# Kernel tuning notes

Measured on AMD Instinct MI355X. Metric: run time of the kernel, lower is better.

## Reference

```python
import jax, jax.numpy as jnp
import numpy as np
from math import sqrt

D_MODEL = 1024
HEADS = 16
D_K = D_MODEL // HEADS
NEG = -1e9


def setup_inputs() -> dict:
    key = jax.random.key(0)
    ks = jax.random.split(key, 8)
    bs, s, d = 2, 2048, D_MODEL
    inp = {
        "k": jax.random.normal(ks[0], (bs, s, d), jnp.float32),
        "v": jax.random.normal(ks[1], (bs, s, d), jnp.float32),
        "q": jax.random.normal(ks[2], (bs, s, d), jnp.float32),
        "mask": jax.random.randint(ks[3], (bs, s, 1), 0, 2).astype(jnp.int64),
        # torch nn.Linear weights: y = x @ W.T, W is [out, in]
        "Wq": jax.random.normal(ks[4], (d, d), jnp.float32) / sqrt(d),
        "Wk": jax.random.normal(ks[5], (d, d), jnp.float32) / sqrt(d),
        "Wv": jax.random.normal(ks[6], (d, d), jnp.float32) / sqrt(d),
        "Wo": jax.random.normal(ks[7], (d, d), jnp.float32) / sqrt(d),
    }
    return inp


def reference(k, v, q, mask, Wq, Wk, Wv, Wo):
    bs, s_k, d = k.shape
    s_q = q.shape[1]
    h, d_k = HEADS, D_K
    # linear projections (no bias), then split heads -> [bs, h, s, d_k]
    kh = (k @ Wk.T).reshape(bs, s_k, h, d_k).transpose(0, 2, 1, 3)
    vh = (v @ Wv.T).reshape(bs, s_k, h, d_k).transpose(0, 2, 1, 3)
    qh = (q @ Wq.T).reshape(bs, s_q, h, d_k).transpose(0, 2, 1, 3)
    # scaled dot-product scores [bs, h, s_q, s_k]
    scores = jnp.einsum("bhqd,bhkd->bhqk", qh, kh) / sqrt(d_k)
    # mask [bs, s_k, 1] -> [bs, 1, 1, s_k], masked positions get -1e9
    m = mask[:, None].transpose(0, 1, 3, 2)  # [bs,1,1,s_k]
    scores = jnp.where(m == 0, NEG, scores)
    probs = jax.nn.softmax(scores, axis=-1)  # dropout is identity (eval)
    attn = jnp.einsum("bhqk,bhkd->bhqd", probs, vh)
    attn_concat = attn.transpose(0, 2, 1, 3).reshape(bs, s_q, d)
    return attn_concat @ Wo.T
```

## Files before the change

### kernel.cpp

```cpp
#include <hip/hip_runtime.h>

typedef __bf16 bf16x8 __attribute__((ext_vector_type(8)));
typedef float f32x4 __attribute__((ext_vector_type(4)));

#define BS 2
#define SEQ 2048
#define DM 1024
#define NH 16
#define DKH 64
#define GM 4096
#define GN 1024
#define GK 1024
#define NEGV (-1e9f)

#define OFF_XQ 0u
#define OFF_XK 4194304u
#define OFF_XV 8388608u
#define OFF_WQ 12582912u
#define OFF_WK 13631488u
#define OFF_WV 14680064u
#define OFF_WO 15728640u
#define OFF_QH 16777216u
#define OFF_KC 20971520u
#define OFF_VT 25165824u
#define OFF_AT OFF_XQ

#if __has_builtin(__builtin_amdgcn_exp2f)
#define EXP2(x) __builtin_amdgcn_exp2f(x)
#else
static __device__ __forceinline__ float EXP2(float x) {
    float r;
    asm volatile("v_exp_f32 %0, %1" : "=v"(r) : "v"(x));
    return r;
}
#endif

__device__ __forceinline__ unsigned cvt_pk(float lo, float hi) {
    unsigned r;
    asm volatile("v_cvt_pk_bf16_f32 %0, %1, %2" : "=v"(r) : "v"(lo), "v"(hi));
    return r;
}

__device__ __forceinline__ unsigned short f2b(float f) {
    unsigned u = __builtin_bit_cast(unsigned, f);
    u += 0x7fffu + ((u >> 16) & 1u);
    return (unsigned short)(u >> 16);
}

typedef const __attribute__((address_space(1))) unsigned int* gas_t;
typedef __attribute__((address_space(3))) unsigned int* las_t;

__device__ __forceinline__ void gload_lds16(const ushort* g, ushort* l) {
    __builtin_amdgcn_global_load_lds((gas_t)(const void*)g, (las_t)(void*)l, 16, 0, 0);
}

__global__ __launch_bounds__(256)
void cvt_kernel(const float* __restrict__ q, const float* __restrict__ k,
                const float* __restrict__ v, const float* __restrict__ wq,
                const float* __restrict__ wk, const float* __restrict__ wv,
                const float* __restrict__ wo, ushort* __restrict__ ws)
{
    const float* src; unsigned n; unsigned dst;
    switch (blockIdx.y) {
        case 0: src = q;  n = 4194304u; dst = OFF_XQ; break;
        case 1: src = k;  n = 4194304u; dst = OFF_XK; break;
        case 2: src = v;  n = 4194304u; dst = OFF_XV; break;
        case 3: src = wq; n = 1048576u; dst = OFF_WQ; break;
        case 4: src = wk; n = 1048576u; dst = OFF_WK; break;
        case 5: src = wv; n = 1048576u; dst = OFF_WV; break;
        default: src = wo; n = 1048576u; dst = OFF_WO; break;
    }
    unsigned i = (blockIdx.x * 256u + threadIdx.x) * 4u;
    if (i >= n) return;
    float4 f = *(const float4*)(src + i);
    ushort4 o;
    o.x = f2b(f.x); o.y = f2b(f.y); o.z = f2b(f.z); o.w = f2b(f.w);
    *(ushort4*)(ws + dst + i) = o;
}

__global__ __launch_bounds__(256)
void scan_kernel(const int* __restrict__ mask, int* __restrict__ cpos, int* __restrict__ mbuf)
{
    const int b = blockIdx.x;
    const int* mp = mask + (size_t)b * SEQ;
    const int tid = threadIdx.x;
    const int lane = tid & 63, w = tid >> 6;
    int v[8];
    int cnt = 0;
#pragma unroll
    for (int j = 0; j < 8; ++j) { v[j] = mp[tid * 8 + j]; cnt += (v[j] != 0); }
    int inc = cnt;
#pragma unroll
    for (int d = 1; d < 64; d <<= 1) {
        int t = __shfl_up(inc, d);
        if (lane >= d) inc += t;
    }
    __shared__ int wsum[4];
    if (lane == 63) wsum[w] = inc;
    __syncthreads();
    int base = inc - cnt;
    for (int i = 0; i < w; ++i) base += wsum[i];
    int c = base;
    int* ob = cpos + (size_t)b * SEQ;
#pragma unroll
    for (int j = 0; j < 8; ++j) {
        ob[tid * 8 + j] = (v[j] != 0) ? c : -1;
        c += (v[j] != 0);
    }
    if (tid == 255) mbuf[b] = base + cnt;
}

template<bool PROJ>
__global__ __launch_bounds__(256)
void gemm_bt(const ushort* __restrict__ Abase, const ushort* __restrict__ Bbase,
             ushort* __restrict__ wsbase, float* __restrict__ of,
             const int* __restrict__ cpos)
{
    __shared__ __align__(16) ushort lA[128 * 64];
    __shared__ __align__(16) ushort lB[128 * 64];

    const ushort* A = Abase;
    const ushort* Bw = Bbase;
    float scale = 1.0f;
    if (PROJ) {
        unsigned z = blockIdx.z;
        A  += (size_t)z * (GM * GK);
        Bw += (size_t)z * (GN * GK);
        if (z == 0) scale = 0.125f * 1.44269504088896f;
    }

    const int tid = threadIdx.x;
    const int lane = tid & 63, wid = tid >> 6;
    const int wr = wid >> 1, wc = wid & 1;
    const int lr = lane & 15, lg = lane >> 4;
    const int lin = blockIdx.y * 8 + blockIdx.x;
    const int swz = (lin & 7) * 32 + (lin >> 3);
    const int m0 = (swz >> 3) * 128, n0 = (swz & 7) * 128;
    const int srow = wid * 32 + (lane >> 3);
    const int scol = (lane & 7) * 8;

    f32x4 acc[4][4] = {};

    for (int k0 = 0; k0 < GK; k0 += 64) {
        __syncthreads();
#pragma unroll
        for (int p = 0; p < 4; ++p) {
            gload_lds16(A + (size_t)(m0 + srow + p * 8) * GK + k0 + scol,
                        &lA[(wid * 32 + p * 8) * 64]);
            gload_lds16(Bw + (size_t)(n0 + srow + p * 8) * GK + k0 + scol,
                        &lB[(wid * 32 + p * 8) * 64]);
        }
        __syncthreads();
#pragma unroll
        for (int kk = 0; kk < 2; ++kk) {
            bf16x8 af[4], bfr[4];
#pragma unroll
            for (int i = 0; i < 4; ++i) {
                af[i]  = *(const bf16x8*)(&lA[(wr * 64 + i * 16 + lr) * 64 + kk * 32 + lg * 8]);
                bfr[i] = *(const bf16x8*)(&lB[(wc * 64 + i * 16 + lr) * 64 + kk * 32 + lg * 8]);
            }
#pragma unroll
            for (int i = 0; i < 4; ++i)
#pragma unroll
                for (int j = 0; j < 4; ++j)
                    acc[i][j] = __builtin_amdgcn_mfma_f32_16x16x32_bf16(af[i], bfr[j], acc[i][j], 0, 0, 0);
        }
    }

    if (PROJ) {
        const int z = blockIdx.z;
        ushort* qh = wsbase + OFF_QH;
        ushort* kc = wsbase + OFF_KC;
        ushort* vtp = wsbase + OFF_VT;
#pragma unroll
        for (int i = 0; i < 4; ++i) {
#pragma unroll
            for (int r = 0; r < 4; ++r) {
                int row = m0 + wr * 64 + i * 16 + lg * 4 + r;
                int b = row >> 11, s = row & 2047;
                if (z == 0) {
#pragma unroll
                    for (int j = 0; j < 4; ++j) {
                        int col = n0 + wc * 64 + j * 16 + lr;
                        qh[(((size_t)b * NH + (col >> 6)) * SEQ + s) * DKH + (col & 63)] =
                            f2b(acc[i][j][r] * scale);
                    }
                } else {
                    int c = cpos[b * SEQ + s];
                    if (c >= 0) {
                        if (z == 1) {
#pragma unroll
                            for (int j = 0; j < 4; ++j) {
                                int col = n0 + wc * 64 + j * 16 + lr;
                                kc[(((size_t)b * NH + (col >> 6)) * SEQ + c) * DKH + (col & 63)] =
                                    f2b(acc[i][j][r]);
                            }
                        } else {
                            int vt = (c & ~63) | ((c & 15) * 4 + ((c >> 4) & 3));
#pragma unroll
                            for (int j = 0; j < 4; ++j) {
                                int col = n0 + wc * 64 + j * 16 + lr;
                                vtp[(((size_t)b * NH + (col >> 6)) * DKH + (col & 63)) * SEQ + vt] =
                                    f2b(acc[i][j][r]);
                            }
                        }
                    }
                }
            }
        }
    } else {
#pragma unroll
        for (int i = 0; i < 4; ++i)
#pragma unroll
            for (int j = 0; j < 4; ++j) {
                int col = n0 + wc * 64 + j * 16 + lr;
#pragma unroll
                for (int r = 0; r < 4; ++r) {
                    int row = m0 + wr * 64 + i * 16 + lg * 4 + r;
                    of[(size_t)row * GN + col] = acc[i][j][r];
                }
            }
    }
}

__global__ __launch_bounds__(256)
void attn_kernel(ushort* __restrict__ ws, const int* __restrict__ mbuf)
{
    const int bid = blockIdx.x;
    const int qt = bid & 31;
    const int h  = (bid >> 5) & 15;
    const int b  = bid >> 9;
    const int bh = b * NH + h;

    const ushort* Qp = ws + OFF_QH + (size_t)bh * (SEQ * DKH);
    const ushort* Kc = ws + OFF_KC + (size_t)bh * (SEQ * DKH);
    const ushort* VT = ws + OFF_VT + (size_t)bh * (DKH * SEQ);
    ushort* At = ws + OFF_AT;

    const int mb = mbuf[b];
    const int nt = (mb + 63) >> 6;

    __shared__ __align__(16) ushort lK[2][64 * 64];
    __shared__ __align__(16) ushort lV[2][64 * 64];
    __shared__ __align__(16) ushort lP[4][16][72];

    const int tid = threadIdx.x;
    const int lane = tid & 63, wid = tid >> 6;
    const int lr = lane & 15, lg = lane >> 4;
    ushort* lPw = &lP[wid][0][0];

    const int srow = wid * 16 + (lane >> 3);
    const int sg = lane & 7;

    const int qrow0 = qt * 64 + wid * 16;
    bf16x8 qf[2];
#pragma unroll
    for (int kk = 0; kk < 2; ++kk)
        qf[kk] = *(const bf16x8*)(Qp + (size_t)(qrow0 + lr) * DKH + kk * 32 + lg * 8);

    f32x4 acc_o[4] = {};
    float lrun[4] = {0.f, 0.f, 0.f, 0.f};

    auto STAGE = [&](int buf, int kt) {
        const int kbase = kt * 64;
#pragma unroll
        for (int c = 0; c < 2; ++c) {
            int r = srow + c * 8;
            gload_lds16(Kc + (size_t)(kbase + r) * DKH + ((sg ^ (r & 7)) * 8),
                        &lK[buf][(wid * 16 + c * 8) * 64]);
            gload_lds16(VT + (size_t)r * SEQ + kbase + ((sg ^ (r & 7)) * 8),
                        &lV[buf][(wid * 16 + c * 8) * 64]);
        }
    };

    STAGE(0, 0);
    __syncthreads();

    for (int kt = 0; kt < nt; ++kt) {
        const int cur = kt & 1;
        if (kt + 1 < nt) STAGE(cur ^ 1, kt + 1);
        const ushort* lKc = lK[cur];
        const ushort* lVc = lV[cur];

        f32x4 s[4];
        __builtin_amdgcn_s_setprio(1);
#pragma unroll
        for (int fc = 0; fc < 4; ++fc) {
            int row = fc * 16 + lr;
            int sw = row & 7;
            bf16x8 kf0 = *(const bf16x8*)(lKc + row * 64 + ((lg ^ sw) * 8));
            bf16x8 kf1 = *(const bf16x8*)(lKc + row * 64 + (((4 + lg) ^ sw) * 8));
            f32x4 t = {};
            t = __builtin_amdgcn_mfma_f32_16x16x32_bf16(qf[0], kf0, t, 0, 0, 0);
            t = __builtin_amdgcn_mfma_f32_16x16x32_bf16(qf[1], kf1, t, 0, 0, 0);
            s[fc] = t;
        }
        __builtin_amdgcn_s_setprio(0);

        if (kt == nt - 1) {
            const int kbase = kt * 64;
#pragma unroll
            for (int fc = 0; fc < 4; ++fc)
                if (kbase + fc * 16 + lr >= mb)
                    s[fc] = f32x4{NEGV, NEGV, NEGV, NEGV};
        }

#pragma unroll
        for (int r = 0; r < 4; ++r) {
            float p0 = EXP2(s[0][r]), p1 = EXP2(s[1][r]);
            float p2 = EXP2(s[2][r]), p3 = EXP2(s[3][r]);
            lrun[r] += (p0 + p1) + (p2 + p3);
            uint2 pk;
            pk.x = cvt_pk(p0, p1);
            pk.y = cvt_pk(p2, p3);
            *(uint2*)(lPw + (lg * 4 + r) * 72 + lr * 4) = pk;
        }

        __builtin_amdgcn_s_setprio(1);
#pragma unroll
        for (int kk = 0; kk < 2; ++kk) {
            bf16x8 pf = *(const bf16x8*)(lPw + lr * 72 + kk * 32 + lg * 8);
#pragma unroll
            for (int fc2 = 0; fc2 < 4; ++fc2) {
                int d = fc2 * 16 + lr;
                bf16x8 vf = *(const bf16x8*)(lVc + d * 64 + (((kk * 4 + lg) ^ (d & 7)) * 8));
                acc_o[fc2] = __builtin_amdgcn_mfma_f32_16x16x32_bf16(pf, vf, acc_o[fc2], 0, 0, 0);
            }
        }
        __builtin_amdgcn_s_setprio(0);
        __syncthreads();
    }

#pragma unroll
    for (int r = 0; r < 4; ++r) {
        float l = lrun[r];
        l += __shfl_xor(l, 1);
        l += __shfl_xor(l, 2);
        l += __shfl_xor(l, 4);
        l += __shfl_xor(l, 8);
        float rl = 1.0f / l;
        int qrow = qrow0 + lg * 4 + r;
#pragma unroll
        for (int fc2 = 0; fc2 < 4; ++fc2)
            At[((size_t)(b * SEQ) + qrow) * DM + h * DKH + fc2 * 16 + lr] =
                f2b(acc_o[fc2][r] * rl);
    }
}

extern "C" void kernel_launch(void* const* d_in, const int* in_sizes, int n_in,
                              void* d_out, int out_size, void* d_ws, size_t ws_size,
                              hipStream_t stream) {
    const float* kin = (const float*)d_in[0];
    const float* vin = (const float*)d_in[1];
    const float* qin = (const float*)d_in[2];
    const int*   msk = (const int*)d_in[3];
    const float* wq  = (const float*)d_in[4];
    const float* wk  = (const float*)d_in[5];
    const float* wv  = (const float*)d_in[6];
    const float* wo  = (const float*)d_in[7];
    ushort* ws = (ushort*)d_ws;
    float* out = (float*)d_out;
    int* cposb = (int*)d_out;
    int* mbuf = cposb + BS * SEQ;

    scan_kernel<<<2, 256, 0, stream>>>(msk, cposb, mbuf);
    cvt_kernel<<<dim3(4096, 7), 256, 0, stream>>>(qin, kin, vin, wq, wk, wv, wo, ws);
    gemm_bt<true><<<dim3(8, 32, 3), 256, 0, stream>>>(ws + OFF_XQ, ws + OFF_WQ, ws, nullptr, cposb);
    attn_kernel<<<1024, 256, 0, stream>>>(ws, mbuf);
    gemm_bt<false><<<dim3(8, 32, 1), 256, 0, stream>>>(ws + OFF_AT, ws + OFF_WO, ws, out, nullptr);
}
```

Before: 141.1 us.

## Replace QKV projection GEMM with 256x256 double-buffered swizzled-LDS pipelined kernel

The batched Q/K/V projection GEMM moves from a 128x128-tile, 256-thread kernel with a single LDS buffer to a 256x256-tile, 512-thread kernel. The new kernel double-buffers LDS, XOR-swizzles the LDS layout to avoid bank conflicts, interleaves global-to-LDS loads with MFMA quadrants under explicit barriers and vmcnt waits, raises wave priority around MFMAs, and remaps blocks per XCD. The goal is to hide load latency and increase operand reuse in the largest GEMM. The cost is much higher LDS and register use per block, only 192 blocks in the grid, and a hand-tuned schedule that depends on the exact order of vmcnt waits.

Measured after the change: 138.3 us. -2.0%, faster.

```diff
diff --git a/kernel.cpp b/kernel.cpp
--- a/kernel.cpp
+++ b/kernel.cpp
@@ -53,6 +53,9 @@
 __device__ __forceinline__ void gload_lds16(const ushort* g, ushort* l) {
     __builtin_amdgcn_global_load_lds((gas_t)(const void*)g, (las_t)(void*)l, 16, 0, 0);
 }
+
+#define BARRIER() do { __builtin_amdgcn_s_barrier(); __builtin_amdgcn_sched_barrier(0); } while (0)
+#define VMCNT(n) do { asm volatile("s_waitcnt vmcnt(" #n ")" ::: "memory"); __builtin_amdgcn_sched_barrier(0); } while (0)
 
 __global__ __launch_bounds__(256)
 void cvt_kernel(const float* __restrict__ q, const float* __restrict__ k,
@@ -110,24 +113,167 @@
     if (tid == 255) mbuf[b] = base + cnt;
 }
 
-template<bool PROJ>
+__global__ __launch_bounds__(512)
+void gemm256(const ushort* __restrict__ Abase, const ushort* __restrict__ Bbase,
+             ushort* __restrict__ wsbase, const int* __restrict__ cpos)
+{
+    __shared__ __align__(16) ushort lA[2][2][8192];
+    __shared__ __align__(16) ushort lB[2][2][8192];
+
+    const unsigned z = blockIdx.z;
+    const ushort* A  = Abase + (size_t)z * (GM * GK);
+    const ushort* Bw = Bbase + (size_t)z * (GN * GK);
+    const float scale = (z == 0) ? 0.125f * 1.44269504088896f : 1.0f;
+
+    const int tid = threadIdx.x;
+    const int lane = tid & 63, wid = tid >> 6;
+    const int wr = wid >> 2, wc = wid & 3;
+    const int lr = lane & 15, lg = lane >> 4;
+    const int srow8 = lane >> 3, scol = lane & 7;
+
+    const int lin = blockIdx.y * 4 + blockIdx.x;
+    const int xcd = lin & 7, kidx = lin >> 3;
+    const int m0 = (xcd * 2 + (kidx >> 2)) * 256;
+    const int n0 = (kidx & 3) * 256;
+
+    f32x4 acc[8][4] = {};
+    bf16x8 aq[4][2], aq2[4][2], b01[2][2], b23[2][2];
+
+#define STAGE_A(s, h, t)                                                          \
+    _Pragma("unroll") for (int c = 0; c < 2; ++c) {                               \
+        int rih = (wid * 2 + c) * 8 + srow8;                                      \
+        gload_lds16(A + (size_t)(m0 + (h) * 128 + rih) * GK + (t) * 64 +          \
+                        ((scol ^ (rih & 7)) * 8),                                 \
+                    &lA[s][h][(wid * 2 + c) * 512]);                              \
+    }
+#define STAGE_B(s, h, t)                                                          \
+    _Pragma("unroll") for (int c = 0; c < 2; ++c) {                               \
+        int rih = (wid * 2 + c) * 8 + srow8;                                      \
+        gload_lds16(Bw + (size_t)(n0 + (h) * 128 + rih) * GK + (t) * 64 +         \
+                         ((scol ^ (rih & 7)) * 8),                                \
+                    &lB[s][h][(wid * 2 + c) * 512]);                              \
+    }
+#define LDA_FRAG(dst, s, ibase)                                                   \
+    _Pragma("unroll") for (int i2 = 0; i2 < 4; ++i2)                              \
+    _Pragma("unroll") for (int kk = 0; kk < 2; ++kk) {                            \
+        int row = ((ibase) + i2) * 16 + lr;                                       \
+        dst[i2][kk] = *(const bf16x8*)&lA[s][wr][row * 64 +                       \
+                          (((kk * 4 + lg) ^ (row & 7)) * 8)];                     \
+    }
+#define LDB_FRAG(dst, s, jbase)                                                   \
+    _Pragma("unroll") for (int j2 = 0; j2 < 2; ++j2)                              \
+    _Pragma("unroll") for (int kk = 0; kk < 2; ++kk) {                            \
+        int row = (wc & 1) * 64 + ((jbase) + j2) * 16 + lr;                       \
+        dst[j2][kk] = *(const bf16x8*)&lB[s][wc >> 1][row * 64 +                  \
+                          (((kk * 4 + lg) ^ (row & 7)) * 8)];                     \
+    }
+#define MMA_Q(ibase, jbase, av, bv)                                               \
+    __builtin_amdgcn_s_setprio(1);                                                \
+    _Pragma("unroll") for (int i2 = 0; i2 < 4; ++i2)                              \
+    _Pragma("unroll") for (int j2 = 0; j2 < 2; ++j2)                              \
+    _Pragma("unroll") for (int kk = 0; kk < 2; ++kk)                              \
+        acc[(ibase) + i2][(jbase) + j2] = __builtin_amdgcn_mfma_f32_16x16x32_bf16(\
+            av[i2][kk], bv[j2][kk], acc[(ibase) + i2][(jbase) + j2], 0, 0, 0);    \
+    __builtin_amdgcn_s_setprio(0);
+
+    STAGE_B(0, 0, 0); STAGE_B(0, 1, 0); STAGE_A(0, 0, 0); STAGE_A(0, 1, 0);
+    STAGE_B(1, 0, 1); STAGE_B(1, 1, 1); STAGE_A(1, 0, 1); STAGE_A(1, 1, 1);
+    VMCNT(8);
+    BARRIER();
+
+    for (int it = 0; it < 7; ++it) {
+        const int t2 = 2 * it + 2, t3 = 2 * it + 3;
+        LDA_FRAG(aq, 0, 0); LDB_FRAG(b01, 0, 0);
+        BARRIER(); MMA_Q(0, 0, aq, b01); BARRIER();
+        LDB_FRAG(b23, 0, 2);
+        BARRIER(); MMA_Q(0, 2, aq, b23); BARRIER();
+        LDA_FRAG(aq2, 0, 4);
+        STAGE_B(0, 0, t2); STAGE_B(0, 1, t2);
+        BARRIER(); MMA_Q(4, 2, aq2, b23); BARRIER();
+        STAGE_A(0, 0, t2);
+        VMCNT(6);
+        BARRIER(); MMA_Q(4, 0, aq2, b01); BARRIER();
+        LDA_FRAG(aq, 1, 0); LDB_FRAG(b01, 1, 0);
+        STAGE_A(0, 1, t2);
+        BARRIER(); MMA_Q(0, 0, aq, b01); BARRIER();
+        LDB_FRAG(b23, 1, 2);
+        BARRIER(); MMA_Q(0, 2, aq, b23); BARRIER();
+        LDA_FRAG(aq2, 1, 4);
+        STAGE_B(1, 0, t3); STAGE_B(1, 1, t3);
+        BARRIER(); MMA_Q(4, 2, aq2, b23); BARRIER();
+        STAGE_A(1, 0, t3); STAGE_A(1, 1, t3);
+        VMCNT(8);
+        BARRIER(); MMA_Q(4, 0, aq2, b01); BARRIER();
+    }
+
+    LDA_FRAG(aq, 0, 0); LDB_FRAG(b01, 0, 0);
+    BARRIER(); MMA_Q(0, 0, aq, b01); BARRIER();
+    LDB_FRAG(b23, 0, 2);
+    BARRIER(); MMA_Q(0, 2, aq, b23); BARRIER();
+    LDA_FRAG(aq2, 0, 4);
+    BARRIER(); MMA_Q(4, 2, aq2, b23); BARRIER();
+    VMCNT(0);
+    BARRIER(); MMA_Q(4, 0, aq2, b01); BARRIER();
+    LDA_FRAG(aq, 1, 0); LDB_FRAG(b01, 1, 0);
+    BARRIER(); MMA_Q(0, 0, aq, b01); BARRIER();
+    LDB_FRAG(b23, 1, 2);
+    BARRIER(); MMA_Q(0, 2, aq, b23); BARRIER();
+    LDA_FRAG(aq2, 1, 4);
+    BARRIER(); MMA_Q(4, 2, aq2, b23); BARRIER();
+    BARRIER(); MMA_Q(4, 0, aq2, b01); BARRIER();
+
+    ushort* qh  = wsbase + OFF_QH;
+    ushort* kc  = wsbase + OFF_KC;
+    ushort* vtp = wsbase + OFF_VT;
+#pragma unroll
+    for (int i = 0; i < 8; ++i) {
+#pragma unroll
+        for (int r = 0; r < 4; ++r) {
+            int row = m0 + wr * 128 + i * 16 + lg * 4 + r;
+            int b = row >> 11, s = row & 2047;
+            if (z == 0) {
+#pragma unroll
+                for (int j = 0; j < 4; ++j) {
+                    int col = n0 + wc * 64 + j * 16 + lr;
+                    qh[(((size_t)b * NH + (col >> 6)) * SEQ + s) * DKH + (col & 63)] =
+                        f2b(acc[i][j][r] * scale);
+                }
+            } else {
+                int c = cpos[b * SEQ + s];
+                if (c >= 0) {
+                    if (z == 1) {
+#pragma unroll
+                        for (int j = 0; j < 4; ++j) {
+                            int col = n0 + wc * 64 + j * 16 + lr;
+                            kc[(((size_t)b * NH + (col >> 6)) * SEQ + c) * DKH + (col & 63)] =
+                                f2b(acc[i][j][r]);
+                        }
+                    } else {
+                        int vt = (c & ~63) | ((c & 15) * 4 + ((c >> 4) & 3));
+#pragma unroll
+                        for (int j = 0; j < 4; ++j) {
+                            int col = n0 + wc * 64 + j * 16 + lr;
+                            vtp[(((size_t)b * NH + (col >> 6)) * DKH + (col & 63)) * SEQ + vt] =
+                                f2b(acc[i][j][r]);
+                        }
+                    }
+                }
+            }
+        }
+    }
+#undef STAGE_A
+#undef STAGE_B
+#undef LDA_FRAG
+#undef LDB_FRAG
+#undef MMA_Q
+}
+
 __global__ __launch_bounds__(256)
-void gemm_bt(const ushort* __restrict__ Abase, const ushort* __restrict__ Bbase,
-             ushort* __restrict__ wsbase, float* __restrict__ of,
-             const int* __restrict__ cpos)
+void gemm_bt(const ushort* __restrict__ A, const ushort* __restrict__ Bw,
+             float* __restrict__ of)
 {
     __shared__ __align__(16) ushort lA[128 * 64];
     __shared__ __align__(16) ushort lB[128 * 64];
-
-    const ushort* A = Abase;
-    const ushort* Bw = Bbase;
-    float scale = 1.0f;
-    if (PROJ) {
-        unsigned z = blockIdx.z;
-        A  += (size_t)z * (GM * GK);
-        Bw += (size_t)z * (GN * GK);
-        if (z == 0) scale = 0.125f * 1.44269504088896f;
-    }
 
     const int tid = threadIdx.x;
     const int lane = tid & 63, wid = tid >> 6;
@@ -167,60 +313,17 @@
         }
     }
 
-    if (PROJ) {
-        const int z = blockIdx.z;
-        ushort* qh = wsbase + OFF_QH;
-        ushort* kc = wsbase + OFF_KC;
-        ushort* vtp = wsbase + OFF_VT;
-#pragma unroll
-        for (int i = 0; i < 4; ++i) {
+#pragma unroll
+    for (int i = 0; i < 4; ++i)
+#pragma unroll
+        for (int j = 0; j < 4; ++j) {
+            int col = n0 + wc * 64 + j * 16 + lr;
 #pragma unroll
             for (int r = 0; r < 4; ++r) {
                 int row = m0 + wr * 64 + i * 16 + lg * 4 + r;
-                int b = row >> 11, s = row & 2047;
-                if (z == 0) {
-#pragma unroll
-                    for (int j = 0; j < 4; ++j) {
-                        int col = n0 + wc * 64 + j * 16 + lr;
-                        qh[(((size_t)b * NH + (col >> 6)) * SEQ + s) * DKH + (col & 63)] =
-                            f2b(acc[i][j][r] * scale);
-                    }
-                } else {
-                    int c = cpos[b * SEQ + s];
-                    if (c >= 0) {
-                        if (z == 1) {
-#pragma unroll
-                            for (int j = 0; j < 4; ++j) {
-                                int col = n0 + wc * 64 + j * 16 + lr;
-                                kc[(((size_t)b * NH + (col >> 6)) * SEQ + c) * DKH + (col & 63)] =
-                                    f2b(acc[i][j][r]);
-                            }
-                        } else {
-                            int vt = (c & ~63) | ((c & 15) * 4 + ((c >> 4) & 3));
-#pragma unroll
-                            for (int j = 0; j < 4; ++j) {
-                                int col = n0 + wc * 64 + j * 16 + lr;
-                                vtp[(((size_t)b * NH + (col >> 6)) * DKH + (col & 63)) * SEQ + vt] =
-                                    f2b(acc[i][j][r]);
-                            }
-                        }
-                    }
-                }
+                of[(size_t)row * GN + col] = acc[i][j][r];
             }
         }
-    } else {
-#pragma unroll
-        for (int i = 0; i < 4; ++i)
-#pragma unroll
-            for (int j = 0; j < 4; ++j) {
-                int col = n0 + wc * 64 + j * 16 + lr;
-#pragma unroll
-                for (int r = 0; r < 4; ++r) {
-                    int row = m0 + wr * 64 + i * 16 + lg * 4 + r;
-                    of[(size_t)row * GN + col] = acc[i][j][r];
-                }
-            }
-    }
 }
 
 __global__ __launch_bounds__(256)
@@ -365,7 +468,7 @@
 
     scan_kernel<<<2, 256, 0, stream>>>(msk, cposb, mbuf);
     cvt_kernel<<<dim3(4096, 7), 256, 0, stream>>>(qin, kin, vin, wq, wk, wv, wo, ws);
-    gemm_bt<true><<<dim3(8, 32, 3), 256, 0, stream>>>(ws + OFF_XQ, ws + OFF_WQ, ws, nullptr, cposb);
+    gemm256<<<dim3(4, 16, 3), 512, 0, stream>>>(ws + OFF_XQ, ws + OFF_WQ, ws, cposb);
     attn_kernel<<<1024, 256, 0, stream>>>(ws, mbuf);
-    gemm_bt<false><<<dim3(8, 32, 1), 256, 0, stream>>>(ws + OFF_AT, ws + OFF_WO, ws, out, nullptr);
-}
+    gemm_bt<<<dim3(8, 32), 256, 0, stream>>>(ws + OFF_AT, ws + OFF_WO, out);
+}
```

## Fuse fp32-to-bf16 conversion into GEMM loads with double-buffered swizzled LDS

Applied to the files above, without the earlier changes.

Removes the separate conversion kernel. The GEMMs now read fp32 activations and weights directly, convert them to bf16 in registers, and write them into XOR-swizzled, double-buffered LDS while the MFMAs run on the other buffer. This drops one kernel launch and a full bf16 round trip through memory. In exchange, each projection block re-reads and re-converts the fp32 weights (re-reading fp32 data that is twice the size of the old bf16 copy), raises register pressure, and uses register-staged loads instead of direct global-to-LDS loads.

After: 196.1 us. 39.0% more time.

```diff
diff --git a/kernel.cpp b/kernel.cpp
--- a/kernel.cpp
+++ b/kernel.cpp
@@ -13,17 +13,10 @@
 #define GK 1024
 #define NEGV (-1e9f)
 
-#define OFF_XQ 0u
-#define OFF_XK 4194304u
-#define OFF_XV 8388608u
-#define OFF_WQ 12582912u
-#define OFF_WK 13631488u
-#define OFF_WV 14680064u
-#define OFF_WO 15728640u
 #define OFF_QH 16777216u
 #define OFF_KC 20971520u
 #define OFF_VT 25165824u
-#define OFF_AT OFF_XQ
+#define OFF_AT 0u
 
 #if __has_builtin(__builtin_amdgcn_exp2f)
 #define EXP2(x) __builtin_amdgcn_exp2f(x)
@@ -52,30 +45,6 @@
 
 __device__ __forceinline__ void gload_lds16(const ushort* g, ushort* l) {
     __builtin_amdgcn_global_load_lds((gas_t)(const void*)g, (las_t)(void*)l, 16, 0, 0);
-}
-
-__global__ __launch_bounds__(256)
-void cvt_kernel(const float* __restrict__ q, const float* __restrict__ k,
-                const float* __restrict__ v, const float* __restrict__ wq,
-                const float* __restrict__ wk, const float* __restrict__ wv,
-                const float* __restrict__ wo, ushort* __restrict__ ws)
-{
-    const float* src; unsigned n; unsigned dst;
-    switch (blockIdx.y) {
-        case 0: src = q;  n = 4194304u; dst = OFF_XQ; break;
-        case 1: src = k;  n = 4194304u; dst = OFF_XK; break;
-        case 2: src = v;  n = 4194304u; dst = OFF_XV; break;
-        case 3: src = wq; n = 1048576u; dst = OFF_WQ; break;
-        case 4: src = wk; n = 1048576u; dst = OFF_WK; break;
-        case 5: src = wv; n = 1048576u; dst = OFF_WV; break;
-        default: src = wo; n = 1048576u; dst = OFF_WO; break;
-    }
-    unsigned i = (blockIdx.x * 256u + threadIdx.x) * 4u;
-    if (i >= n) return;
-    float4 f = *(const float4*)(src + i);
-    ushort4 o;
-    o.x = f2b(f.x); o.y = f2b(f.y); o.z = f2b(f.z); o.w = f2b(f.w);
-    *(ushort4*)(ws + dst + i) = o;
 }
 
 __global__ __launch_bounds__(256)
@@ -111,22 +80,26 @@
 }
 
 template<bool PROJ>
-__global__ __launch_bounds__(256)
-void gemm_bt(const ushort* __restrict__ Abase, const ushort* __restrict__ Bbase,
-             ushort* __restrict__ wsbase, float* __restrict__ of,
-             const int* __restrict__ cpos)
+__global__ __launch_bounds__(256, 2)
+void gemm_fused(const float* __restrict__ qin, const float* __restrict__ kin,
+                const float* __restrict__ vin, const float* __restrict__ wqp,
+                const float* __restrict__ wkp, const float* __restrict__ wvp,
+                const float* __restrict__ wop, ushort* __restrict__ ws,
+                float* __restrict__ of, const int* __restrict__ cpos)
 {
-    __shared__ __align__(16) ushort lA[128 * 64];
-    __shared__ __align__(16) ushort lB[128 * 64];
-
-    const ushort* A = Abase;
-    const ushort* Bw = Bbase;
-    float scale = 1.0f;
+    __shared__ __align__(16) ushort lA[2][128 * 64];
+    __shared__ __align__(16) ushort lB[2][128 * 64];
+
+    const int z = PROJ ? blockIdx.z : 0;
+    const float* Af = nullptr;
+    const ushort* Ab = nullptr;
+    const float* Bf;
     if (PROJ) {
-        unsigned z = blockIdx.z;
-        A  += (size_t)z * (GM * GK);
-        Bw += (size_t)z * (GN * GK);
-        if (z == 0) scale = 0.125f * 1.44269504088896f;
+        Af = (z == 0) ? qin : (z == 1) ? kin : vin;
+        Bf = (z == 0) ? wqp : (z == 1) ? wkp : wvp;
+    } else {
+        Ab = ws + OFF_AT;
+        Bf = wop;
     }
 
     const int tid = threadIdx.x;
@@ -136,28 +109,67 @@
     const int lin = blockIdx.y * 8 + blockIdx.x;
     const int swz = (lin & 7) * 32 + (lin >> 3);
     const int m0 = (swz >> 3) * 128, n0 = (swz & 7) * 128;
-    const int srow = wid * 32 + (lane >> 3);
-    const int scol = (lane & 7) * 8;
+    const int srow = tid >> 1, sch = tid & 1;
+    const int swb = srow & 7;
 
     f32x4 acc[4][4] = {};
-
-    for (int k0 = 0; k0 < GK; k0 += 64) {
-        __syncthreads();
-#pragma unroll
-        for (int p = 0; p < 4; ++p) {
-            gload_lds16(A + (size_t)(m0 + srow + p * 8) * GK + k0 + scol,
-                        &lA[(wid * 32 + p * 8) * 64]);
-            gload_lds16(Bw + (size_t)(n0 + srow + p * 8) * GK + k0 + scol,
-                        &lB[(wid * 32 + p * 8) * 64]);
-        }
-        __syncthreads();
+    float4 ar[8], br[8];
+    uint4 arb[4];
+
+    auto LOAD = [&](int t) {
+        const int k0 = t * 64;
+        if (PROJ) {
+#pragma unroll
+            for (int m = 0; m < 8; ++m)
+                ar[m] = *(const float4*)(Af + (size_t)(m0 + srow) * GK + k0 + sch * 32 + m * 4);
+        } else {
+#pragma unroll
+            for (int m = 0; m < 4; ++m)
+                arb[m] = *(const uint4*)(Ab + (size_t)(m0 + srow) * GK + k0 + sch * 32 + m * 8);
+        }
+#pragma unroll
+        for (int m = 0; m < 8; ++m)
+            br[m] = *(const float4*)(Bf + (size_t)(n0 + srow) * GK + k0 + sch * 32 + m * 4);
+    };
+
+    auto WRITE = [&](int s) {
+#pragma unroll
+        for (int m = 0; m < 4; ++m) {
+            uint4 w;
+            if (PROJ) {
+                w.x = cvt_pk(ar[2 * m].x, ar[2 * m].y);
+                w.y = cvt_pk(ar[2 * m].z, ar[2 * m].w);
+                w.z = cvt_pk(ar[2 * m + 1].x, ar[2 * m + 1].y);
+                w.w = cvt_pk(ar[2 * m + 1].z, ar[2 * m + 1].w);
+            } else {
+                w = arb[m];
+            }
+            *(uint4*)&lA[s][srow * 64 + (((sch * 4 + m) ^ swb) * 8)] = w;
+            uint4 wb;
+            wb.x = cvt_pk(br[2 * m].x, br[2 * m].y);
+            wb.y = cvt_pk(br[2 * m].z, br[2 * m].w);
+            wb.z = cvt_pk(br[2 * m + 1].x, br[2 * m + 1].y);
+            wb.w = cvt_pk(br[2 * m + 1].z, br[2 * m + 1].w);
+            *(uint4*)&lB[s][srow * 64 + (((sch * 4 + m) ^ swb) * 8)] = wb;
+        }
+    };
+
+    LOAD(0);
+    WRITE(0);
+    __syncthreads();
+
+    for (int t = 0; t < 16; ++t) {
+        const int cur = t & 1;
+        if (t < 15) LOAD(t + 1);
 #pragma unroll
         for (int kk = 0; kk < 2; ++kk) {
             bf16x8 af[4], bfr[4];
 #pragma unroll
             for (int i = 0; i < 4; ++i) {
-                af[i]  = *(const bf16x8*)(&lA[(wr * 64 + i * 16 + lr) * 64 + kk * 32 + lg * 8]);
-                bfr[i] = *(const bf16x8*)(&lB[(wc * 64 + i * 16 + lr) * 64 + kk * 32 + lg * 8]);
+                const int rowa = wr * 64 + i * 16 + lr;
+                af[i]  = *(const bf16x8*)&lA[cur][rowa * 64 + (((kk * 4 + lg) ^ (rowa & 7)) * 8)];
+                const int rowb = wc * 64 + i * 16 + lr;
+                bfr[i] = *(const bf16x8*)&lB[cur][rowb * 64 + (((kk * 4 + lg) ^ (rowb & 7)) * 8)];
             }
 #pragma unroll
             for (int i = 0; i < 4; ++i)
@@ -165,13 +177,15 @@
                 for (int j = 0; j < 4; ++j)
                     acc[i][j] = __builtin_amdgcn_mfma_f32_16x16x32_bf16(af[i], bfr[j], acc[i][j], 0, 0, 0);
         }
+        if (t < 15) WRITE(cur ^ 1);
+        __syncthreads();
     }
 
     if (PROJ) {
-        const int z = blockIdx.z;
-        ushort* qh = wsbase + OFF_QH;
-        ushort* kc = wsbase + OFF_KC;
-        ushort* vtp = wsbase + OFF_VT;
+        const float scale = (z == 0) ? 0.125f * 1.44269504088896f : 1.0f;
+        ushort* qh  = ws + OFF_QH;
+        ushort* kc  = ws + OFF_KC;
+        ushort* vtp = ws + OFF_VT;
 #pragma unroll
         for (int i = 0; i < 4; ++i) {
 #pragma unroll
@@ -364,8 +378,9 @@
     int* mbuf = cposb + BS * SEQ;
 
     scan_kernel<<<2, 256, 0, stream>>>(msk, cposb, mbuf);
-    cvt_kernel<<<dim3(4096, 7), 256, 0, stream>>>(qin, kin, vin, wq, wk, wv, wo, ws);
-    gemm_bt<true><<<dim3(8, 32, 3), 256, 0, stream>>>(ws + OFF_XQ, ws + OFF_WQ, ws, nullptr, cposb);
+    gemm_fused<true><<<dim3(8, 32, 3), 256, 0, stream>>>(qin, kin, vin, wq, wk, wv, wo,
+                                                         ws, nullptr, cposb);
     attn_kernel<<<1024, 256, 0, stream>>>(ws, mbuf);
-    gemm_bt<false><<<dim3(8, 32, 1), 256, 0, stream>>>(ws + OFF_AT, ws + OFF_WO, ws, out, nullptr);
-}
+    gemm_fused<false><<<dim3(8, 32, 1), 256, 0, stream>>>(qin, kin, vin, wq, wk, wv, wo,
+                                                          ws, out, nullptr);
+}
```
